# Optimization experiments

Hardware: AMD Instinct MI355X
Metric: run time of the kernel (lower is better)

The kernel has to match this reference:

```python
import jax, jax.numpy as jnp
import numpy as np

B, L, C = 16, 3136, 96
H_, W_ = 56, 56
R = 3            # graph relations (short/medium/long range)
CTX = 2          # context relations: depthwise convs with kernels 3 and 5 (use_all_context)
RT = R + CTX
E = 131072
FFN_H = 4 * C


def setup_inputs() -> dict:
    key = jax.random.key(0)
    ks = jax.random.split(key, 16)
    s = lambda i, shape: jax.random.normal(ks[i], shape, dtype=jnp.float32) * 0.02
    return {
        "x": jax.random.normal(ks[0], (B, L, C), dtype=jnp.float32),
        "edge_index": jax.random.randint(ks[1], (2, E), 0, L),
        "edge_type": jax.random.randint(ks[2], (E,), 0, R),
        "H": H_, "W": W_,
        "norm1_g": jnp.ones((C,), jnp.float32), "norm1_b": jnp.zeros((C,), jnp.float32),
        "value_w": s(3, (C, C)), "value_b": jnp.zeros((C,), jnp.float32),
        "gate_w": s(4, (C, RT)), "gate_b": jnp.zeros((RT,), jnp.float32),
        "ctx_k3": s(5, (C, 1, 3, 3)), "ctx_b3": jnp.zeros((C,), jnp.float32),
        "ctx_k5": s(6, (C, 1, 5, 5)), "ctx_b5": jnp.zeros((C,), jnp.float32),
        "rel_w": s(7, (RT * C, C)), "rel_b": jnp.zeros((C,), jnp.float32),
        "proj_w": s(8, (C, C)), "proj_b": jnp.zeros((C,), jnp.float32),
        "norm2_g": jnp.ones((C,), jnp.float32), "norm2_b": jnp.zeros((C,), jnp.float32),
        "fc1_w": s(9, (C, FFN_H)), "fc1_b": jnp.zeros((FFN_H,), jnp.float32),
        "fc2_w": s(10, (FFN_H, C)), "fc2_b": jnp.zeros((C,), jnp.float32),
    }


def layer_norm(x, g, b, eps=1e-5):
    mu = x.mean(-1, keepdims=True)
    var = ((x - mu) ** 2).mean(-1, keepdims=True)
    return (x - mu) * jax.lax.rsqrt(var + eps) * g + b


def dwconv(x_bchw, k, b):
    out = jax.lax.conv_general_dilated(
        x_bchw, k, window_strides=(1, 1), padding="SAME",
        feature_group_count=x_bchw.shape[1],
        dimension_numbers=("NCHW", "OIHW", "NCHW"))
    return out + b[None, :, None, None]


def grmp(x, edge_index, edge_type, H, W,
         value_w, value_b, gate_w, gate_b,
         ctx_k3, ctx_b3, ctx_k5, ctx_b5, rel_w, rel_b):
    # Gated relational message passing over RT relations.
    Bx, Lx, Cx = x.shape
    v = x @ value_w + value_b                               # [B,L,C] node values
    src, dst = edge_index[0], edge_index[1]
    seg = dst * R + edge_type                               # fused (node, relation) segment id
    cnt = jax.ops.segment_sum(jnp.ones((E,), x.dtype), seg, num_segments=Lx * R)
    cnt = jnp.maximum(cnt, 1.0)[None, :, None]
    # mean-aggregate messages per (dst node, relation)
    agg = jax.vmap(lambda vb: jax.ops.segment_sum(vb[src], seg, num_segments=Lx * R))(v)
    agg = (agg / cnt).reshape(Bx, Lx, R, Cx)                # [B,L,R,C]
    # context relations: depthwise convs on the spatial layout of values
    v_img = v.reshape(Bx, H, W, Cx).transpose(0, 3, 1, 2)   # [B,C,H,W]
    c3 = dwconv(v_img, ctx_k3, ctx_b3).transpose(0, 2, 3, 1).reshape(Bx, Lx, 1, Cx)
    c5 = dwconv(v_img, ctx_k5, ctx_b5).transpose(0, 2, 3, 1).reshape(Bx, Lx, 1, Cx)
    upd = jnp.concatenate([agg, c3, c5], axis=2)            # [B,L,RT,C]
    gate = jax.nn.sigmoid(x @ gate_w + gate_b)              # [B,L,RT] per-relation gates
    upd = upd * gate[..., None]
    out = upd.reshape(Bx, Lx, RT * Cx) @ rel_w + rel_b      # relation mixing
    return jax.nn.gelu(out, approximate=False)


def reference(x, edge_index, edge_type, H, W,
              norm1_g, norm1_b, value_w, value_b, gate_w, gate_b,
              ctx_k3, ctx_b3, ctx_k5, ctx_b5, rel_w, rel_b,
              proj_w, proj_b, norm2_g, norm2_b, fc1_w, fc1_b, fc2_w, fc2_b):
    h = layer_norm(x, norm1_g, norm1_b)
    h = grmp(h, edge_index, edge_type, H, W, value_w, value_b, gate_w, gate_b,
             ctx_k3, ctx_b3, ctx_k5, ctx_b5, rel_w, rel_b)
    h = h @ proj_w + proj_b
    x = x + h                                               # residual 1 (drop_path = identity)
    h2 = layer_norm(x, norm2_g, norm2_b)
    h2 = jax.nn.gelu(h2 @ fc1_w + fc1_b, approximate=False) @ fc2_w + fc2_b
    return x + h2                                           # residual 2
```

## Files before the change

### kernel.cpp

```cpp
#include <hip/hip_runtime.h>
#include <hip/hip_bf16.h>
#include <math.h>

#define BB 16
#define LL 3136
#define CC 96
#define HH 56
#define WW 56
#define RR 3
#define RTOT 5
#define EE 131072
#define NR (BB*LL)
#define NSEG (LL*RR)
#define FFN 384

typedef __attribute__((ext_vector_type(8))) short bf16x8;
typedef __attribute__((ext_vector_type(4))) float f32x4;
typedef __attribute__((ext_vector_type(8))) unsigned short u16x8;

__device__ __forceinline__ unsigned short f2bf(float f) {
    unsigned u = __builtin_bit_cast(unsigned, f);
    unsigned r = u + 0x7FFF + ((u >> 16) & 1);
    return (unsigned short)(r >> 16);
}
__device__ __forceinline__ float bf2f(unsigned short h) {
    unsigned u = ((unsigned)h) << 16;
    return __builtin_bit_cast(float, u);
}

__device__ __forceinline__ float gelu_exact(float v) {
    return 0.5f * v * (1.0f + erff(v * 0.70710678118654752440f));
}

__global__ __launch_bounds__(256) void ln_kernel(const float* __restrict__ x,
                                                 const float* __restrict__ g,
                                                 const float* __restrict__ bta,
                                                 float* __restrict__ out, int nrows)
{
    int wave = threadIdx.x >> 6;
    int lane = threadIdx.x & 63;
    int row  = blockIdx.x * 4 + wave;
    if (row >= nrows) return;
    const float* xr = x + (size_t)row * CC;
    float v0 = xr[lane];
    float v1 = (lane < 32) ? xr[64 + lane] : 0.f;
    float s = v0 + v1;
    #pragma unroll
    for (int off = 32; off; off >>= 1) s += __shfl_xor(s, off);
    float mean = s * (1.f / 96.f);
    float d0 = v0 - mean;
    float d1 = (lane < 32) ? (v1 - mean) : 0.f;
    float q = d0 * d0 + d1 * d1;
    #pragma unroll
    for (int off = 32; off; off >>= 1) q += __shfl_xor(q, off);
    float rstd = rsqrtf(q * (1.f / 96.f) + 1e-5f);
    out[(size_t)row * CC + lane] = d0 * rstd * g[lane] + bta[lane];
    if (lane < 32)
        out[(size_t)row * CC + 64 + lane] = d1 * rstd * g[64 + lane] + bta[64 + lane];
}

#define SPL_TOT 138240
__global__ __launch_bounds__(256) void prep_split(const float* __restrict__ vw,
                                                  const float* __restrict__ rw,
                                                  const float* __restrict__ pw,
                                                  const float* __restrict__ f1w,
                                                  const float* __restrict__ f2w,
                                                  unsigned short* __restrict__ bhi,
                                                  unsigned short* __restrict__ blo)
{
    int t = blockIdx.x * 256 + threadIdx.x;
    if (t >= SPL_TOT) return;
    const float* src; int K, N, local;
    if (t < 9216)        { src = vw;  K = 96;  N = 96;  local = t; }
    else if (t < 55296)  { src = rw;  K = 480; N = 96;  local = t - 9216; }
    else if (t < 64512)  { src = pw;  K = 96;  N = 96;  local = t - 55296; }
    else if (t < 101376) { src = f1w; K = 96;  N = 384; local = t - 64512; }
    else                 { src = f2w; K = 384; N = 96;  local = t - 101376; }
    int n = local / K, k = local - n * K;
    float f = src[(size_t)k * N + n];
    unsigned short h = f2bf(f);
    unsigned short l = f2bf(f - bf2f(h));
    bhi[t] = h;
    blo[t] = l;
}

template<int ACT, bool RES, bool PERM>
__global__ __launch_bounds__(256) void gemm_mfma(const float* __restrict__ A,
                                                 const unsigned short* __restrict__ Bhi,
                                                 const unsigned short* __restrict__ Blo,
                                                 const float* __restrict__ bias,
                                                 const float* __restrict__ res,
                                                 float* __restrict__ out,
                                                 int M, int N, int K)
{
    __shared__ unsigned short AsH[64 * 32], AsL[64 * 32];
    __shared__ unsigned short BsH[96 * 32], BsL[96 * 32];
    const int tid  = threadIdx.x;
    const int bm   = blockIdx.x * 64;
    const int bn   = blockIdx.y * 96;
    const int lane = tid & 63;
    const int w    = tid >> 6;
    const int wm   = w >> 1, wn = w & 1;
    const int r16  = lane & 15, q = lane >> 4;

    f32x4 acc[2][3];
    #pragma unroll
    for (int mt = 0; mt < 2; mt++)
        #pragma unroll
        for (int nt = 0; nt < 3; nt++) acc[mt][nt] = (f32x4)0.f;

    const int arow = tid >> 2;
    const int akq  = (tid & 3) * 8;
    const int bn_  = tid >> 1;
    const int bh_  = (tid & 1) * 16;

    for (int kc = 0; kc < K; kc += 32) {
        __syncthreads();
        {
            const float* ap = A + (size_t)(bm + arow) * K + kc + akq;
            float4 f0 = *(const float4*)ap;
            float4 f1 = *(const float4*)(ap + 4);
            float ff[8] = {f0.x, f0.y, f0.z, f0.w, f1.x, f1.y, f1.z, f1.w};
            u16x8 h8, l8;
            #pragma unroll
            for (int j = 0; j < 8; j++) {
                unsigned short h = f2bf(ff[j]);
                h8[j] = h;
                l8[j] = f2bf(ff[j] - bf2f(h));
            }
            *(u16x8*)&AsH[arow * 32 + akq] = h8;
            *(u16x8*)&AsL[arow * 32 + akq] = l8;
        }
        if (tid < 192) {
            const unsigned short* bph = Bhi + (size_t)(bn + bn_) * K + kc + bh_;
            const unsigned short* bpl = Blo + (size_t)(bn + bn_) * K + kc + bh_;
            u16x8 h0 = *(const u16x8*)bph;
            u16x8 h1 = *(const u16x8*)(bph + 8);
            u16x8 l0 = *(const u16x8*)bpl;
            u16x8 l1 = *(const u16x8*)(bpl + 8);
            *(u16x8*)&BsH[bn_ * 32 + bh_ + 0] = h0;
            *(u16x8*)&BsH[bn_ * 32 + bh_ + 8] = h1;
            *(u16x8*)&BsL[bn_ * 32 + bh_ + 0] = l0;
            *(u16x8*)&BsL[bn_ * 32 + bh_ + 8] = l1;
        }
        __syncthreads();
        bf16x8 aH[2], aL[2], bH[3], bL[3];
        #pragma unroll
        for (int mt = 0; mt < 2; mt++) {
            int rbase = (wm * 32 + mt * 16 + r16) * 32 + q * 8;
            aH[mt] = *(const bf16x8*)&AsH[rbase];
            aL[mt] = *(const bf16x8*)&AsL[rbase];
        }
        #pragma unroll
        for (int nt = 0; nt < 3; nt++) {
            int cbase = (wn * 48 + nt * 16 + r16) * 32 + q * 8;
            bH[nt] = *(const bf16x8*)&BsH[cbase];
            bL[nt] = *(const bf16x8*)&BsL[cbase];
        }
        #pragma unroll
        for (int mt = 0; mt < 2; mt++)
            #pragma unroll
            for (int nt = 0; nt < 3; nt++) {
                acc[mt][nt] = __builtin_amdgcn_mfma_f32_16x16x32_bf16(aH[mt], bH[nt], acc[mt][nt], 0, 0, 0);
                acc[mt][nt] = __builtin_amdgcn_mfma_f32_16x16x32_bf16(aH[mt], bL[nt], acc[mt][nt], 0, 0, 0);
                acc[mt][nt] = __builtin_amdgcn_mfma_f32_16x16x32_bf16(aL[mt], bH[nt], acc[mt][nt], 0, 0, 0);
            }
    }

    #pragma unroll
    for (int mt = 0; mt < 2; mt++) {
        #pragma unroll
        for (int nt = 0; nt < 3; nt++) {
            int col = bn + wn * 48 + nt * 16 + r16;
            float bv = bias[col];
            #pragma unroll
            for (int r = 0; r < 4; r++) {
                int row = bm + wm * 32 + mt * 16 + q * 4 + r;
                float val = acc[mt][nt][r] + bv;
                if (ACT == 1) val = gelu_exact(val);
                if (RES) val += res[(size_t)row * N + col];
                size_t orow;
                if (PERM) {
                    int b = row / LL;
                    int l = row - b * LL;
                    orow = (size_t)l * BB + b;
                } else {
                    orow = (size_t)row;
                }
                out[orow * N + col] = val;
            }
        }
    }
}

__global__ __launch_bounds__(256) void gate_kernel(const float* __restrict__ h,
                                                   const float* __restrict__ gw,
                                                   const float* __restrict__ gb,
                                                   float* __restrict__ gate)
{
    int wave = threadIdx.x >> 6;
    int lane = threadIdx.x & 63;
    int row  = blockIdx.x * 4 + wave;
    if (row >= NR) return;
    const float* hr = h + (size_t)row * CC;
    float v0 = hr[lane];
    float v1 = (lane < 32) ? hr[64 + lane] : 0.f;
    #pragma unroll
    for (int r = 0; r < RTOT; r++) {
        float s = v0 * gw[lane * RTOT + r];
        if (lane < 32) s += v1 * gw[(64 + lane) * RTOT + r];
        #pragma unroll
        for (int off = 32; off; off >>= 1) s += __shfl_xor(s, off);
        if (lane == r) gate[(size_t)row * RTOT + r] = 1.f / (1.f + expf(-(s + gb[r])));
    }
}

__global__ void hist_kernel(const int* __restrict__ ei, const int* __restrict__ et,
                            int* __restrict__ cnt)
{
    int e = blockIdx.x * 256 + threadIdx.x;
    if (e >= EE) return;
    int dst = ei[EE + e];
    int r   = et[e];
    atomicAdd(&cnt[dst * RR + r], 1);
}

__global__ __launch_bounds__(1024) void scan_kernel(const int* __restrict__ cnt,
                                                    int* __restrict__ colptr,
                                                    float* __restrict__ invcnt)
{
    __shared__ int wsum[16];
    int tid = threadIdx.x, wid = tid >> 6, lane = tid & 63;
    int carry = 0;
    for (int base = 0; base < NSEG; base += 1024) {
        int idx = base + tid;
        int v = (idx < NSEG) ? cnt[idx] : 0;
        if (idx < NSEG) invcnt[idx] = 1.f / (float)max(v, 1);
        int sc = v;
        #pragma unroll
        for (int off = 1; off < 64; off <<= 1) {
            int o = __shfl_up(sc, off);
            if (lane >= off) sc += o;
        }
        if (lane == 63) wsum[wid] = sc;
        __syncthreads();
        if (wid == 0) {
            int w = (lane < 16) ? wsum[lane] : 0;
            #pragma unroll
            for (int off = 1; off < 16; off <<= 1) {
                int o = __shfl_up(w, off);
                if (lane >= off) w += o;
            }
            if (lane < 16) wsum[lane] = w;
        }
        __syncthreads();
        int woff = (wid > 0) ? wsum[wid - 1] : 0;
        if (idx < NSEG) colptr[idx] = carry + woff + sc - v;
        carry += wsum[15];
        __syncthreads();
    }
    if (tid == 0) colptr[NSEG] = carry;
}

__global__ void scatter_kernel(const int* __restrict__ ei, const int* __restrict__ et,
                               const int* __restrict__ colptr, int* __restrict__ fill,
                               int* __restrict__ esorted)
{
    int e = blockIdx.x * 256 + threadIdx.x;
    if (e >= EE) return;
    int src = ei[e];
    int dst = ei[EE + e];
    int seg = dst * RR + et[e];
    int pos = colptr[seg] + atomicAdd(&fill[seg], 1);
    esorted[pos] = src;
}

__global__ __launch_bounds__(96) void aggconv_kernel(const float* __restrict__ vp,
                               const float* __restrict__ gate,
                               const int* __restrict__ colptr, const int* __restrict__ esorted,
                               const float* __restrict__ invcnt,
                               const float* __restrict__ k3, const float* __restrict__ b3,
                               const float* __restrict__ k5, const float* __restrict__ b5,
                               float* __restrict__ updg)
{
    int l = blockIdx.x;
    int c = threadIdx.x;
    __shared__ float gs[BB][RTOT];
    if (c < BB * RTOT) {
        int b = c / RTOT, r = c - b * RTOT;
        gs[b][r] = gate[((size_t)b * LL + l) * RTOT + r];
    }
    __syncthreads();

    #pragma unroll
    for (int r = 0; r < RR; r++) {
        int s0 = colptr[l * RR + r], s1 = colptr[l * RR + r + 1];
        float acc[BB];
        #pragma unroll
        for (int b = 0; b < BB; b++) acc[b] = 0.f;
        int src = (s0 < s1) ? esorted[s0] : 0;
        for (int e = s0; e < s1; e++) {
            int nsrc = (e + 1 < s1) ? esorted[e + 1] : 0;
            const float* p = vp + (size_t)src * (BB * CC) + c;
            #pragma unroll
            for (int b = 0; b < BB; b++) acc[b] += p[b * CC];
            src = nsrc;
        }
        float inv = invcnt[l * RR + r];
        #pragma unroll
        for (int b = 0; b < BB; b++)
            updg[((size_t)b * LL + l) * (RTOT * CC) + r * CC + c] = acc[b] * inv * gs[b][r];
    }

    int h0 = l / WW, w0 = l - (l / WW) * WW;
    float a3[BB], a5[BB];
    float bb3 = b3[c], bb5 = b5[c];
    #pragma unroll
    for (int b = 0; b < BB; b++) { a3[b] = bb3; a5[b] = bb5; }
    #pragma unroll
    for (int kh = -2; kh <= 2; kh++) {
        int hh = h0 + kh; if (hh < 0 || hh >= HH) continue;
        #pragma unroll
        for (int kw = -2; kw <= 2; kw++) {
            int ww = w0 + kw; if (ww < 0 || ww >= WW) continue;
            float w5 = k5[c * 25 + (kh + 2) * 5 + (kw + 2)];
            bool in3 = (kh >= -1 && kh <= 1 && kw >= -1 && kw <= 1);
            float w3 = in3 ? k3[c * 9 + (kh + 1) * 3 + (kw + 1)] : 0.f;
            const float* p = vp + (size_t)(hh * WW + ww) * (BB * CC) + c;
            #pragma unroll
            for (int b = 0; b < BB; b++) {
                float t = p[b * CC];
                a5[b] += t * w5;
                a3[b] += t * w3;
            }
        }
    }
    #pragma unroll
    for (int b = 0; b < BB; b++) {
        size_t ob = ((size_t)b * LL + l) * (RTOT * CC);
        updg[ob + 3 * CC + c] = a3[b] * gs[b][3];
        updg[ob + 4 * CC + c] = a5[b] * gs[b][4];
    }
}

extern "C" void kernel_launch(void* const* d_in, const int* in_sizes, int n_in,
                              void* d_out, int out_size, void* d_ws, size_t ws_size,
                              hipStream_t stream)
{
    const float* x       = (const float*)d_in[0];
    const int*   ei      = (const int*)d_in[1];
    const int*   et      = (const int*)d_in[2];
    const float* n1g     = (const float*)d_in[5];
    const float* n1b     = (const float*)d_in[6];
    const float* value_w = (const float*)d_in[7];
    const float* value_b = (const float*)d_in[8];
    const float* gate_w  = (const float*)d_in[9];
    const float* gate_b  = (const float*)d_in[10];
    const float* k3      = (const float*)d_in[11];
    const float* b3      = (const float*)d_in[12];
    const float* k5      = (const float*)d_in[13];
    const float* b5      = (const float*)d_in[14];
    const float* rel_w   = (const float*)d_in[15];
    const float* rel_b   = (const float*)d_in[16];
    const float* proj_w  = (const float*)d_in[17];
    const float* proj_b  = (const float*)d_in[18];
    const float* n2g     = (const float*)d_in[19];
    const float* n2b     = (const float*)d_in[20];
    const float* fc1_w   = (const float*)d_in[21];
    const float* fc1_b   = (const float*)d_in[22];
    const float* fc2_w   = (const float*)d_in[23];
    const float* fc2_b   = (const float*)d_in[24];
    float* out = (float*)d_out;

    float* w = (float*)d_ws;
    const size_t SZ_ROW = (size_t)NR * CC;
    float* hbuf   = w;
    float* vbuf   = hbuf + SZ_ROW;
    float* gateb  = vbuf + SZ_ROW;
    float* updg   = gateb + (size_t)NR * RTOT;
    int*   ibase  = (int*)(updg + (size_t)NR * RTOT * CC);
    int*   cnt     = ibase;
    int*   colptr  = cnt + NSEG;
    int*   fill    = colptr + NSEG + 1;
    int*   esorted = fill + NSEG;
    float* invcnt  = (float*)(esorted + EE);
    unsigned short* bhi = (unsigned short*)(invcnt + NSEG);
    unsigned short* blo = bhi + SPL_TOT;

    hipMemsetAsync(cnt, 0, NSEG * sizeof(int), stream);
    hipMemsetAsync(fill, 0, NSEG * sizeof(int), stream);

    prep_split<<<(SPL_TOT + 255) / 256, 256, 0, stream>>>(value_w, rel_w, proj_w, fc1_w, fc2_w, bhi, blo);
    ln_kernel<<<NR / 4, 256, 0, stream>>>(x, n1g, n1b, hbuf, NR);
    gemm_mfma<0, false, true><<<dim3(NR / 64, 1), 256, 0, stream>>>(hbuf, bhi + 0, blo + 0, value_b, nullptr, vbuf, NR, 96, 96);
    gate_kernel<<<NR / 4, 256, 0, stream>>>(hbuf, gate_w, gate_b, gateb);
    hist_kernel<<<EE / 256, 256, 0, stream>>>(ei, et, cnt);
    scan_kernel<<<1, 1024, 0, stream>>>(cnt, colptr, invcnt);
    scatter_kernel<<<EE / 256, 256, 0, stream>>>(ei, et, colptr, fill, esorted);
    aggconv_kernel<<<dim3(LL), 96, 0, stream>>>(vbuf, gateb, colptr, esorted, invcnt,
                                                k3, b3, k5, b5, updg);
    gemm_mfma<1, false, false><<<dim3(NR / 64, 1), 256, 0, stream>>>(updg, bhi + 9216, blo + 9216, rel_b, nullptr, hbuf, NR, 96, 480);
    gemm_mfma<0, true, false><<<dim3(NR / 64, 1), 256, 0, stream>>>(hbuf, bhi + 55296, blo + 55296, proj_b, x, vbuf, NR, 96, 96);
    ln_kernel<<<NR / 4, 256, 0, stream>>>(vbuf, n2g, n2b, hbuf, NR);
    gemm_mfma<1, false, false><<<dim3(NR / 64, 4), 256, 0, stream>>>(hbuf, bhi + 64512, blo + 64512, fc1_b, nullptr, updg, NR, 384, 96);
    gemm_mfma<0, true, false><<<dim3(NR / 64, 1), 256, 0, stream>>>(updg, bhi + 101376, blo + 101376, fc2_b, vbuf, out, NR, 96, 384);
}
```

Before: 451.5 us.

## Store intermediate activations in bf16 and regroup aggconv threads by batch

Intermediate activations (values, relation updates, GRMP output, FFN hidden) are now written and read as bf16 instead of fp32. GEMMs that consume bf16 A operands skip the hi/lo split and drop one of the three MFMA passes. The aggregation/conv kernel is rewritten to 256 threads, each handling one batch and six channels with packed bf16 loads, using pre-transposed conv weights. This cuts memory traffic and MFMA work at the cost of lower precision in the intermediates, which could affect accuracy tolerance.

```diff
diff --git a/kernel.cpp b/kernel.cpp
--- a/kernel.cpp
+++ b/kernel.cpp
@@ -84,16 +84,33 @@
     blo[t] = l;
 }
 
-template<int ACT, bool RES, bool PERM>
-__global__ __launch_bounds__(256) void gemm_mfma(const float* __restrict__ A,
+__global__ __launch_bounds__(256) void prep_convw(const float* __restrict__ k3,
+                                                  const float* __restrict__ k5,
+                                                  float* __restrict__ k3t,
+                                                  float* __restrict__ k5t)
+{
+    int t = blockIdx.x * 256 + threadIdx.x;
+    if (t < 864) {
+        int c = t / 9, tap = t - c * 9;
+        k3t[tap * 96 + c] = k3[t];
+    } else if (t < 864 + 2400) {
+        int u = t - 864;
+        int c = u / 25, tap = u - c * 25;
+        k5t[tap * 96 + c] = k5[u];
+    }
+}
+
+template<int ACT, bool RES, bool PERM, bool ABF16, bool OUTBF16>
+__global__ __launch_bounds__(256) void gemm_mfma(const void* __restrict__ Ain,
                                                  const unsigned short* __restrict__ Bhi,
                                                  const unsigned short* __restrict__ Blo,
                                                  const float* __restrict__ bias,
                                                  const float* __restrict__ res,
-                                                 float* __restrict__ out,
+                                                 void* __restrict__ outv,
                                                  int M, int N, int K)
 {
-    __shared__ unsigned short AsH[64 * 32], AsL[64 * 32];
+    __shared__ unsigned short AsH[64 * 32];
+    __shared__ unsigned short AsL[ABF16 ? 8 : 64 * 32];
     __shared__ unsigned short BsH[96 * 32], BsL[96 * 32];
     const int tid  = threadIdx.x;
     const int bm   = blockIdx.x * 64;
@@ -116,7 +133,12 @@
 
     for (int kc = 0; kc < K; kc += 32) {
         __syncthreads();
-        {
+        if constexpr (ABF16) {
+            const unsigned short* Ab = (const unsigned short*)Ain;
+            u16x8 h8 = *(const u16x8*)&Ab[(size_t)(bm + arow) * K + kc + akq];
+            *(u16x8*)&AsH[arow * 32 + akq] = h8;
+        } else {
+            const float* A = (const float*)Ain;
             const float* ap = A + (size_t)(bm + arow) * K + kc + akq;
             float4 f0 = *(const float4*)ap;
             float4 f1 = *(const float4*)(ap + 4);
@@ -149,7 +171,7 @@
         for (int mt = 0; mt < 2; mt++) {
             int rbase = (wm * 32 + mt * 16 + r16) * 32 + q * 8;
             aH[mt] = *(const bf16x8*)&AsH[rbase];
-            aL[mt] = *(const bf16x8*)&AsL[rbase];
+            if constexpr (!ABF16) aL[mt] = *(const bf16x8*)&AsL[rbase];
         }
         #pragma unroll
         for (int nt = 0; nt < 3; nt++) {
@@ -163,7 +185,8 @@
             for (int nt = 0; nt < 3; nt++) {
                 acc[mt][nt] = __builtin_amdgcn_mfma_f32_16x16x32_bf16(aH[mt], bH[nt], acc[mt][nt], 0, 0, 0);
                 acc[mt][nt] = __builtin_amdgcn_mfma_f32_16x16x32_bf16(aH[mt], bL[nt], acc[mt][nt], 0, 0, 0);
-                acc[mt][nt] = __builtin_amdgcn_mfma_f32_16x16x32_bf16(aL[mt], bH[nt], acc[mt][nt], 0, 0, 0);
+                if constexpr (!ABF16)
+                    acc[mt][nt] = __builtin_amdgcn_mfma_f32_16x16x32_bf16(aL[mt], bH[nt], acc[mt][nt], 0, 0, 0);
             }
     }
 
@@ -187,7 +210,10 @@
                 } else {
                     orow = (size_t)row;
                 }
-                out[orow * N + col] = val;
+                if constexpr (OUTBF16)
+                    ((unsigned short*)outv)[orow * N + col] = f2bf(val);
+                else
+                    ((float*)outv)[orow * N + col] = val;
             }
         }
     }
@@ -275,72 +301,101 @@
     esorted[pos] = src;
 }
 
-__global__ __launch_bounds__(96) void aggconv_kernel(const float* __restrict__ vp,
-                               const float* __restrict__ gate,
-                               const int* __restrict__ colptr, const int* __restrict__ esorted,
-                               const float* __restrict__ invcnt,
-                               const float* __restrict__ k3, const float* __restrict__ b3,
-                               const float* __restrict__ k5, const float* __restrict__ b5,
-                               float* __restrict__ updg)
+__device__ __forceinline__ void unp6(const unsigned short* p, float* f) {
+    unsigned u0 = *(const unsigned*)(p + 0);
+    unsigned u1 = *(const unsigned*)(p + 2);
+    unsigned u2 = *(const unsigned*)(p + 4);
+    f[0] = bf2f((unsigned short)u0); f[1] = bf2f((unsigned short)(u0 >> 16));
+    f[2] = bf2f((unsigned short)u1); f[3] = bf2f((unsigned short)(u1 >> 16));
+    f[4] = bf2f((unsigned short)u2); f[5] = bf2f((unsigned short)(u2 >> 16));
+}
+__device__ __forceinline__ void pack6(unsigned short* p, const float* f) {
+    unsigned u0 = (unsigned)f2bf(f[0]) | ((unsigned)f2bf(f[1]) << 16);
+    unsigned u1 = (unsigned)f2bf(f[2]) | ((unsigned)f2bf(f[3]) << 16);
+    unsigned u2 = (unsigned)f2bf(f[4]) | ((unsigned)f2bf(f[5]) << 16);
+    *(unsigned*)(p + 0) = u0;
+    *(unsigned*)(p + 2) = u1;
+    *(unsigned*)(p + 4) = u2;
+}
+
+__global__ __launch_bounds__(256) void aggconv_kernel(
+        const unsigned short* __restrict__ vp,
+        const float* __restrict__ gate,
+        const int* __restrict__ colptr, const int* __restrict__ esorted,
+        const float* __restrict__ invcnt,
+        const float* __restrict__ k3t, const float* __restrict__ b3,
+        const float* __restrict__ k5t, const float* __restrict__ b5,
+        unsigned short* __restrict__ updg)
 {
     int l = blockIdx.x;
-    int c = threadIdx.x;
-    __shared__ float gs[BB][RTOT];
-    if (c < BB * RTOT) {
-        int b = c / RTOT, r = c - b * RTOT;
-        gs[b][r] = gate[((size_t)b * LL + l) * RTOT + r];
-    }
-    __syncthreads();
+    int t = threadIdx.x;
+    int b = t >> 4;
+    int g = t & 15;
+    int ch = g * 6;
+
+    float gs[RTOT];
+    #pragma unroll
+    for (int r = 0; r < RTOT; r++) gs[r] = gate[((size_t)b * LL + l) * RTOT + r];
+    size_t ob = ((size_t)b * LL + l) * (RTOT * CC);
 
     #pragma unroll
     for (int r = 0; r < RR; r++) {
         int s0 = colptr[l * RR + r], s1 = colptr[l * RR + r + 1];
-        float acc[BB];
-        #pragma unroll
-        for (int b = 0; b < BB; b++) acc[b] = 0.f;
+        float acc[6] = {0.f, 0.f, 0.f, 0.f, 0.f, 0.f};
         int src = (s0 < s1) ? esorted[s0] : 0;
         for (int e = s0; e < s1; e++) {
             int nsrc = (e + 1 < s1) ? esorted[e + 1] : 0;
-            const float* p = vp + (size_t)src * (BB * CC) + c;
-            #pragma unroll
-            for (int b = 0; b < BB; b++) acc[b] += p[b * CC];
+            float f[6];
+            unp6(vp + ((size_t)src * BB + b) * CC + ch, f);
+            #pragma unroll
+            for (int j = 0; j < 6; j++) acc[j] += f[j];
             src = nsrc;
         }
-        float inv = invcnt[l * RR + r];
-        #pragma unroll
-        for (int b = 0; b < BB; b++)
-            updg[((size_t)b * LL + l) * (RTOT * CC) + r * CC + c] = acc[b] * inv * gs[b][r];
+        float sc = invcnt[l * RR + r] * gs[r];
+        float o[6];
+        #pragma unroll
+        for (int j = 0; j < 6; j++) o[j] = acc[j] * sc;
+        unsigned short ov[6];
+        pack6(ov, o);
+        *(unsigned*)(updg + ob + r * CC + ch + 0) = *(unsigned*)(ov + 0);
+        *(unsigned*)(updg + ob + r * CC + ch + 2) = *(unsigned*)(ov + 2);
+        *(unsigned*)(updg + ob + r * CC + ch + 4) = *(unsigned*)(ov + 4);
     }
 
     int h0 = l / WW, w0 = l - (l / WW) * WW;
-    float a3[BB], a5[BB];
-    float bb3 = b3[c], bb5 = b5[c];
-    #pragma unroll
-    for (int b = 0; b < BB; b++) { a3[b] = bb3; a5[b] = bb5; }
+    float a3[6], a5[6];
+    #pragma unroll
+    for (int j = 0; j < 6; j++) { a3[j] = b3[ch + j]; a5[j] = b5[ch + j]; }
     #pragma unroll
     for (int kh = -2; kh <= 2; kh++) {
         int hh = h0 + kh; if (hh < 0 || hh >= HH) continue;
         #pragma unroll
         for (int kw = -2; kw <= 2; kw++) {
             int ww = w0 + kw; if (ww < 0 || ww >= WW) continue;
-            float w5 = k5[c * 25 + (kh + 2) * 5 + (kw + 2)];
-            bool in3 = (kh >= -1 && kh <= 1 && kw >= -1 && kw <= 1);
-            float w3 = in3 ? k3[c * 9 + (kh + 1) * 3 + (kw + 1)] : 0.f;
-            const float* p = vp + (size_t)(hh * WW + ww) * (BB * CC) + c;
-            #pragma unroll
-            for (int b = 0; b < BB; b++) {
-                float t = p[b * CC];
-                a5[b] += t * w5;
-                a3[b] += t * w3;
+            float f[6];
+            unp6(vp + ((size_t)(hh * WW + ww) * BB + b) * CC + ch, f);
+            int tap5 = (kh + 2) * 5 + (kw + 2);
+            #pragma unroll
+            for (int j = 0; j < 6; j++) a5[j] += f[j] * k5t[tap5 * CC + ch + j];
+            if (kh >= -1 && kh <= 1 && kw >= -1 && kw <= 1) {
+                int tap3 = (kh + 1) * 3 + (kw + 1);
+                #pragma unroll
+                for (int j = 0; j < 6; j++) a3[j] += f[j] * k3t[tap3 * CC + ch + j];
             }
         }
     }
-    #pragma unroll
-    for (int b = 0; b < BB; b++) {
-        size_t ob = ((size_t)b * LL + l) * (RTOT * CC);
-        updg[ob + 3 * CC + c] = a3[b] * gs[b][3];
-        updg[ob + 4 * CC + c] = a5[b] * gs[b][4];
-    }
+    float o3[6], o5[6];
+    #pragma unroll
+    for (int j = 0; j < 6; j++) { o3[j] = a3[j] * gs[3]; o5[j] = a5[j] * gs[4]; }
+    unsigned short v3[6], v5[6];
+    pack6(v3, o3);
+    pack6(v5, o5);
+    *(unsigned*)(updg + ob + 3 * CC + ch + 0) = *(unsigned*)(v3 + 0);
+    *(unsigned*)(updg + ob + 3 * CC + ch + 2) = *(unsigned*)(v3 + 2);
+    *(unsigned*)(updg + ob + 3 * CC + ch + 4) = *(unsigned*)(v3 + 4);
+    *(unsigned*)(updg + ob + 4 * CC + ch + 0) = *(unsigned*)(v5 + 0);
+    *(unsigned*)(updg + ob + 4 * CC + ch + 2) = *(unsigned*)(v5 + 2);
+    *(unsigned*)(updg + ob + 4 * CC + ch + 4) = *(unsigned*)(v5 + 4);
 }
 
 extern "C" void kernel_launch(void* const* d_in, const int* in_sizes, int n_in,
@@ -386,22 +441,31 @@
     float* invcnt  = (float*)(esorted + EE);
     unsigned short* bhi = (unsigned short*)(invcnt + NSEG);
     unsigned short* blo = bhi + SPL_TOT;
+    float* k3t = (float*)(blo + SPL_TOT);
+    float* k5t = k3t + 864;
+
+    unsigned short* vp_bf   = (unsigned short*)vbuf;
+    unsigned short* g1_bf   = (unsigned short*)hbuf;
+    unsigned short* updg_bf = (unsigned short*)updg;
+    unsigned short* hid_bf  = (unsigned short*)updg;
+    float* x1 = vbuf;
 
     hipMemsetAsync(cnt, 0, NSEG * sizeof(int), stream);
     hipMemsetAsync(fill, 0, NSEG * sizeof(int), stream);
 
     prep_split<<<(SPL_TOT + 255) / 256, 256, 0, stream>>>(value_w, rel_w, proj_w, fc1_w, fc2_w, bhi, blo);
+    prep_convw<<<(864 + 2400 + 255) / 256, 256, 0, stream>>>(k3, k5, k3t, k5t);
     ln_kernel<<<NR / 4, 256, 0, stream>>>(x, n1g, n1b, hbuf, NR);
-    gemm_mfma<0, false, true><<<dim3(NR / 64, 1), 256, 0, stream>>>(hbuf, bhi + 0, blo + 0, value_b, nullptr, vbuf, NR, 96, 96);
+    gemm_mfma<0, false, true, false, true><<<dim3(NR / 64, 1), 256, 0, stream>>>(hbuf, bhi + 0, blo + 0, value_b, nullptr, vp_bf, NR, 96, 96);
     gate_kernel<<<NR / 4, 256, 0, stream>>>(hbuf, gate_w, gate_b, gateb);
     hist_kernel<<<EE / 256, 256, 0, stream>>>(ei, et, cnt);
     scan_kernel<<<1, 1024, 0, stream>>>(cnt, colptr, invcnt);
     scatter_kernel<<<EE / 256, 256, 0, stream>>>(ei, et, colptr, fill, esorted);
-    aggconv_kernel<<<dim3(LL), 96, 0, stream>>>(vbuf, gateb, colptr, esorted, invcnt,
-                                                k3, b3, k5, b5, updg);
-    gemm_mfma<1, false, false><<<dim3(NR / 64, 1), 256, 0, stream>>>(updg, bhi + 9216, blo + 9216, rel_b, nullptr, hbuf, NR, 96, 480);
-    gemm_mfma<0, true, false><<<dim3(NR / 64, 1), 256, 0, stream>>>(hbuf, bhi + 55296, blo + 55296, proj_b, x, vbuf, NR, 96, 96);
-    ln_kernel<<<NR / 4, 256, 0, stream>>>(vbuf, n2g, n2b, hbuf, NR);
-    gemm_mfma<1, false, false><<<dim3(NR / 64, 4), 256, 0, stream>>>(hbuf, bhi + 64512, blo + 64512, fc1_b, nullptr, updg, NR, 384, 96);
-    gemm_mfma<0, true, false><<<dim3(NR / 64, 1), 256, 0, stream>>>(updg, bhi + 101376, blo + 101376, fc2_b, vbuf, out, NR, 96, 384);
-}
+    aggconv_kernel<<<dim3(LL), 256, 0, stream>>>(vp_bf, gateb, colptr, esorted, invcnt,
+                                                 k3t, b3, k5t, b5, updg_bf);
+    gemm_mfma<1, false, false, true, true><<<dim3(NR / 64, 1), 256, 0, stream>>>(updg_bf, bhi + 9216, blo + 9216, rel_b, nullptr, g1_bf, NR, 96, 480);
+    gemm_mfma<0, true, false, true, false><<<dim3(NR / 64, 1), 256, 0, stream>>>(g1_bf, bhi + 55296, blo + 55296, proj_b, x, x1, NR, 96, 96);
+    ln_kernel<<<NR / 4, 256, 0, stream>>>(x1, n2g, n2b, hbuf, NR);
+    gemm_mfma<1, false, false, false, true><<<dim3(NR / 64, 4), 256, 0, stream>>>(hbuf, bhi + 64512, blo + 64512, fc1_b, nullptr, hid_bf, NR, 384, 96);
+    gemm_mfma<0, true, false, true, false><<<dim3(NR / 64, 1), 256, 0, stream>>>(hid_bf, bhi + 101376, blo + 101376, fc2_b, x1, out, NR, 96, 384);
+}
```

Measured after the change: 379.1 us. 16.0% less time.
